# Performance work log

Measured on AMD Instinct MI355X. Metric: run time of the kernel, lower is better.

## Reference

```python
import jax, jax.numpy as jnp
import numpy as np

MARGIN = 1.0   # TripletLoss(margin) init arg
EPS = 1e-6     # torch F.pairwise_distance eps used by nn.TripletMarginLoss
INF = 1e9

N, D_EMB, N_CLASSES = 8192, 1024, 128


def setup_inputs() -> dict:
    key = jax.random.key(0)
    k1, k2 = jax.random.split(key)
    embeddings = jax.random.normal(k1, (N, D_EMB), dtype=jnp.float32)
    target = jax.random.randint(k2, (N,), 0, N_CLASSES, dtype=jnp.int64 if jax.config.jax_enable_x64 else jnp.int32)
    return {"embeddings": embeddings, "target": target}


def _mine_and_loss(embeddings, target):
    # Vectorized, deterministic equivalent of the per-anchor random mining loop:
    # full pairwise L2 distance matrix via a GEMM (compute-bound core).
    sq = jnp.sum(embeddings * embeddings, axis=1)                      # [N]
    d2 = sq[:, None] + sq[None, :] - 2.0 * (embeddings @ embeddings.T)  # [N, N]
    Dm = jnp.sqrt(jnp.maximum(d2, 0.0))                                 # [N, N]

    same = target[:, None] == target[None, :]
    eye = jnp.eye(target.shape[0], dtype=bool)
    pos_mask = same & ~eye          # valid positives (same class, not self)
    neg_mask = ~same                # valid negatives (different class)

    # Positive: hardest (farthest) same-class sample (deterministic stand-in
    # for the original's random positive draw).
    pos_scores = jnp.where(pos_mask, Dm, -INF)
    pos_idx = jnp.argmax(pos_scores, axis=1)                           # [N]
    d_p = jnp.max(pos_scores, axis=1)                                  # [N]

    # Negative: semi-hard (d_p < d_n < d_p + margin), pick the closest such
    # negative; if none exists, fall back to the overall hardest (min-dist)
    # negative -- mirrors the loop's early-break vs. min_dist fallback.
    semi = neg_mask & (Dm > d_p[:, None]) & (Dm < (d_p + MARGIN)[:, None])
    has_semi = jnp.any(semi, axis=1)
    neg_semi = jnp.argmin(jnp.where(semi, Dm, INF), axis=1)
    neg_hard = jnp.argmin(jnp.where(neg_mask, Dm, INF), axis=1)
    neg_idx = jnp.where(has_semi, neg_semi, neg_hard)                  # [N]

    # nn.TripletMarginLoss(margin, p=2): mean(relu(d(a,p) - d(a,n) + margin))
    # with torch's pairwise_distance eps added to the difference.
    a = embeddings
    p = embeddings[pos_idx]
    n = embeddings[neg_idx]
    dp = jnp.sqrt(jnp.sum((a - p + EPS) ** 2, axis=1))
    dn = jnp.sqrt(jnp.sum((a - n + EPS) ** 2, axis=1))
    return jnp.mean(jax.nn.relu(dp - dn + MARGIN))


def reference(embeddings, target):
    return _mine_and_loss(embeddings, target)
```

## Files before the change

### kernel.cpp

```cpp
#include <hip/hip_runtime.h>
#include <hip/hip_bf16.h>

#define N 8192
#define D 1024
#define MARGIN 1.0f
#define EPS 1e-6f

typedef __attribute__((ext_vector_type(8))) short bf16x8;
typedef __attribute__((ext_vector_type(4))) float f32x4;
typedef __attribute__((ext_vector_type(8))) _Float16 f16x8;
typedef __attribute__((ext_vector_type(4))) _Float16 f16x4;
typedef __attribute__((ext_vector_type(8))) unsigned short u16x8;

__device__ inline unsigned short f2bf(float x) {
    unsigned u = __float_as_uint(x);
    unsigned r = (u + 0x7FFFu + ((u >> 16) & 1u)) >> 16;
    return (unsigned short)r;
}

__device__ inline float h2f(unsigned hb) {
    return (float)__builtin_bit_cast(_Float16, (unsigned short)hb);
}

__global__ __launch_bounds__(256) void prep_kernel(const float* __restrict__ E,
                                                   const int* __restrict__ target,
                                                   unsigned short* __restrict__ Ebf,
                                                   float* __restrict__ sq,
                                                   unsigned char* __restrict__ cls) {
    const int tid = threadIdx.x;
    const int lane = tid & 63, wave = tid >> 6;
    const int r = blockIdx.x * 4 + wave;
    const float4 v = ((const float4*)(E + (size_t)r * D))[lane];
    ushort4 o;
    o.x = f2bf(v.x); o.y = f2bf(v.y); o.z = f2bf(v.z); o.w = f2bf(v.w);
    ((ushort4*)(Ebf + (size_t)r * D))[lane] = o;
    float s = v.x * v.x + v.y * v.y + v.z * v.z + v.w * v.w;
    for (int off = 32; off > 0; off >>= 1) s += __shfl_down(s, off);
    if (lane == 0) {
        sq[r] = s;
        cls[r] = (unsigned char)target[r];
    }
}


#define SLOT_0A0 0
#define SLOT_0A1 16384
#define SLOT_0B0 32768
#define SLOT_0B1 49152
#define SLOT_1A0 65536
#define SLOT_1A1 81920
#define SLOT_1B0 98304
#define SLOT_1B1 114688

#define VMW(n) __asm__ __volatile__("s_waitcnt vmcnt(" #n ")" ::: "memory")
#define NOSTAGE ((void)0)
#define NOWAIT ((void)0)

#define STAGE(slotOff, baseRow, kcol) do {                                              \
    const unsigned short* _s0 = E + (size_t)((baseRow) + (tid >> 2)) * D + (kcol) + stc * 8; \
    __builtin_amdgcn_global_load_lds(                                                    \
        (const __attribute__((address_space(1))) unsigned int*)_s0,                      \
        (__attribute__((address_space(3))) unsigned int*)(smem + (slotOff) + wave * 1024), 16, 0, 0); \
    const unsigned short* _s1 = _s0 + (size_t)128 * D;                                   \
    __builtin_amdgcn_global_load_lds(                                                    \
        (const __attribute__((address_space(1))) unsigned int*)_s1,                      \
        (__attribute__((address_space(3))) unsigned int*)(smem + (slotOff) + 8192 + wave * 1024), 16, 0, 0); \
} while (0)

#define PHASE(b, ks, mq, LOADB, STG, WAIT) do {                                          \
    const char* _As = smem + (b) * 65536 + (ks) * 16384;                                 \
    const char* _Bs = smem + (b) * 65536 + 32768 + (ks) * 16384;                         \
    if (LOADB) {                                                                         \
        _Pragma("unroll") for (int nj = 0; nj < 4; ++nj)                                 \
            bfr[nj] = *(const bf16x8*)(_Bs + (wn * 64 + nj * 16 + mr) * 64 + swz);       \
    }                                                                                    \
    bf16x8 af[4];                                                                        \
    _Pragma("unroll") for (int mi = 0; mi < 4; ++mi)                                     \
        af[mi] = *(const bf16x8*)(_As + (wm * 128 + (mq) * 64 + mi * 16 + mr) * 64 + swz); \
    STG;                                                                                 \
    __builtin_amdgcn_s_setprio(1);                                                       \
    _Pragma("unroll") for (int mi = 0; mi < 4; ++mi)                                     \
        _Pragma("unroll") for (int nj = 0; nj < 4; ++nj)                                 \
            acc[(mq) * 4 + mi][nj] = __builtin_amdgcn_mfma_f32_16x16x32_bf16(            \
                af[mi], bfr[nj], acc[(mq) * 4 + mi][nj], 0, 0, 0);                       \
    __builtin_amdgcn_s_setprio(0);                                                       \
    WAIT;                                                                                \
    __asm__ __volatile__("s_barrier" ::: "memory");                                      \
} while (0)

__device__ __forceinline__ void diag_path(char* smem,
                                          const unsigned short* __restrict__ E,
                                          const float* __restrict__ sq,
                                          _Float16* __restrict__ D2h,
                                          const int c, const int tid) {
    const int lane = tid & 63;
    const int wave = tid >> 6;
    const int wmL = wave >> 2;
    const int wnL = wave & 3;
    const int mr = lane & 15;
    const int q = lane >> 4;
    const int kq = q * 8;

    const int t = c / 3, s = c - 3 * t;
    const int smi = (s + 1) >> 1;
    const int sni = s >> 1;
    const int rm = t * 256 + smi * 128;
    const int cn = t * 256 + sni * 128;
    const bool offdiag = (s == 1);

    f32x4 acc[4][2] = {};

#define DSTAGE(sl, kk) do {                                                              \
    __builtin_amdgcn_global_load_lds(                                                    \
        (const __attribute__((address_space(1))) unsigned int*)(E + (size_t)(rm + (tid >> 2)) * D + (kk) * 32 + (tid & 3) * 8), \
        (__attribute__((address_space(3))) unsigned int*)(smem + (sl) * 32768 + wave * 1024), 16, 0, 0); \
    __builtin_amdgcn_global_load_lds(                                                    \
        (const __attribute__((address_space(1))) unsigned int*)(E + (size_t)(cn + (tid >> 2)) * D + (kk) * 32 + (tid & 3) * 8), \
        (__attribute__((address_space(3))) unsigned int*)(smem + (sl) * 32768 + 16384 + wave * 1024), 16, 0, 0); \
} while (0)

#define DCOMPUTE(k) do {                                                                 \
    const unsigned short* As = (const unsigned short*)(smem + (size_t)((k) & 3) * 32768);\
    const unsigned short* Bs = As + 8192;                                                \
    bf16x8 af[4], bfv[2];                                                                \
    _Pragma("unroll") for (int mi = 0; mi < 4; ++mi)                                     \
        af[mi] = *(const bf16x8*)(As + (wmL * 64 + mi * 16 + mr) * 32 + kq);             \
    _Pragma("unroll") for (int ni = 0; ni < 2; ++ni)                                     \
        bfv[ni] = *(const bf16x8*)(Bs + (wnL * 32 + ni * 16 + mr) * 32 + kq);            \
    _Pragma("unroll") for (int mi = 0; mi < 4; ++mi)                                     \
        _Pragma("unroll") for (int ni = 0; ni < 2; ++ni)                                 \
            acc[mi][ni] = __builtin_amdgcn_mfma_f32_16x16x32_bf16(af[mi], bfv[ni], acc[mi][ni], 0, 0, 0); \
} while (0)

    DSTAGE(0, 0);
    DSTAGE(1, 1);
    for (int k = 0; k < 30; ++k) {
        DSTAGE((k + 2) & 3, k + 2);
        __asm__ __volatile__("s_waitcnt vmcnt(4)" ::: "memory");
        __asm__ __volatile__("s_barrier" ::: "memory");
        DCOMPUTE(k);
    }
    __asm__ __volatile__("s_waitcnt vmcnt(2)" ::: "memory");
    __asm__ __volatile__("s_barrier" ::: "memory");
    DCOMPUTE(30);
    __asm__ __volatile__("s_waitcnt vmcnt(0)" ::: "memory");
    __asm__ __volatile__("s_barrier" ::: "memory");
    DCOMPUTE(31);
#undef DSTAGE
#undef DCOMPUTE
    __syncthreads();

    _Float16* Ts = (_Float16*)smem;
    float sqjL[2];
#pragma unroll
    for (int ni = 0; ni < 2; ++ni) sqjL[ni] = sq[cn + wnL * 32 + ni * 16 + mr];
#pragma unroll
    for (int mi = 0; mi < 4; ++mi) {
        const int lrow = wmL * 64 + mi * 16 + q * 4;
        const int i0 = rm + lrow;
        const f32x4 sqi = *(const f32x4*)(sq + i0);
#pragma unroll
        for (int ni = 0; ni < 2; ++ni) {
            const int lcol = wnL * 32 + ni * 16 + mr;
            const int j = cn + lcol;
            f16x4 tv;
#pragma unroll
            for (int r = 0; r < 4; ++r) {
                const float d2 = fmaxf(sqi[r] + sqjL[ni] - 2.0f * acc[mi][ni][r], 0.0f);
                const _Float16 h = (_Float16)d2;
                D2h[(size_t)(i0 + r) * N + j] = h;
                tv[r] = h;
            }
            if (offdiag)
                *(f16x4*)(Ts + (size_t)lcol * 136 + lrow) = tv;
        }
    }
    if (offdiag) {
        __syncthreads();
#pragma unroll
        for (int it = 0; it < 4; ++it) {
            const int rt = it * 32 + (tid >> 4);
            const int seg = tid & 15;
            f16x8 v = *(const f16x8*)(Ts + (size_t)rt * 136 + seg * 8);
            *(f16x8*)(D2h + (size_t)(cn + rt) * N + rm + seg * 8) = v;
        }
    }
}

__global__ __launch_bounds__(512, 2) void gemm_kernel(const unsigned short* __restrict__ E,
                                                      const float* __restrict__ sq,
                                                      _Float16* __restrict__ D2h) {
    extern __shared__ char smem[];

    const int tid = threadIdx.x;

    if (blockIdx.x >= 496) {
        diag_path(smem, E, sq, D2h, blockIdx.x - 496, tid);
        return;
    }

    const int lane = tid & 63;
    const int wave = tid >> 6;
    const int wm = wave >> 2;
    const int wn = wave & 3;
    const int mr = lane & 15;
    const int q = lane >> 4;
    const int swz = ((q ^ ((mr >> 1) & 3)) << 4);
    const int stc = (tid & 3) ^ ((tid >> 3) & 3);

    const int h = blockIdx.x;
    const int l = (h & 7) * 62 + (h >> 3);
    int by = (int)((1.0f + sqrtf(8.0f * (float)l + 1.0f)) * 0.5f);
    while (by * (by - 1) / 2 > l) --by;
    while ((by + 1) * by / 2 <= l) ++by;
    const int bx = l - by * (by - 1) / 2;
    const int rm = by * 256;
    const int cn = bx * 256;

    f32x4 acc[8][4] = {};
    bf16x8 bfr[4];

    STAGE(SLOT_0A0, rm, 0);
    STAGE(SLOT_0B0, cn, 0);
    STAGE(SLOT_0A1, rm, 32);
    STAGE(SLOT_0B1, cn, 32);
    STAGE(SLOT_1A0, rm, 64);
    VMW(6);
    __asm__ __volatile__("s_barrier" ::: "memory");

    for (int i = 0; i < 7; ++i) {
        const int kt = 2 * i;
        PHASE(0, 0, 0, 1, STAGE(SLOT_1B0, cn, (kt + 1) * 64 + 0),  NOWAIT);
        PHASE(0, 0, 1, 0, STAGE(SLOT_1A1, rm, (kt + 1) * 64 + 32), VMW(6));
        PHASE(0, 1, 0, 1, STAGE(SLOT_1B1, cn, (kt + 1) * 64 + 32), NOWAIT);
        PHASE(0, 1, 1, 0, STAGE(SLOT_0A0, rm, (kt + 2) * 64 + 0),  VMW(6));
        PHASE(1, 0, 0, 1, STAGE(SLOT_0B0, cn, (kt + 2) * 64 + 0),  NOWAIT);
        PHASE(1, 0, 1, 0, STAGE(SLOT_0A1, rm, (kt + 2) * 64 + 32), VMW(6));
        PHASE(1, 1, 0, 1, STAGE(SLOT_0B1, cn, (kt + 2) * 64 + 32), NOWAIT);
        PHASE(1, 1, 1, 0, STAGE(SLOT_1A0, rm, (kt + 3) * 64 + 0),  VMW(6));
    }
    PHASE(0, 0, 0, 1, STAGE(SLOT_1B0, cn, 15 * 64 + 0),  NOWAIT);
    PHASE(0, 0, 1, 0, STAGE(SLOT_1A1, rm, 15 * 64 + 32), VMW(6));
    PHASE(0, 1, 0, 1, STAGE(SLOT_1B1, cn, 15 * 64 + 32), NOWAIT);
    PHASE(0, 1, 1, 0, NOSTAGE, VMW(4));
    PHASE(1, 0, 0, 1, NOSTAGE, NOWAIT);
    PHASE(1, 0, 1, 0, NOSTAGE, VMW(0));
    PHASE(1, 1, 0, 1, NOSTAGE, NOWAIT);
    PHASE(1, 1, 1, 0, NOSTAGE, NOWAIT);

    __asm__ __volatile__("s_waitcnt lgkmcnt(0)" ::: "memory");
    __asm__ __volatile__("s_barrier" ::: "memory");

    const int crow = q * 4;
    float sqj[4];
#pragma unroll
    for (int nj = 0; nj < 4; ++nj) sqj[nj] = sq[cn + wn * 64 + nj * 16 + mr];
    float sqiv[8][4];
#pragma unroll
    for (int mg = 0; mg < 8; ++mg) {
        const f32x4 s4 = *(const f32x4*)(sq + rm + wm * 128 + mg * 16 + crow);
#pragma unroll
        for (int r = 0; r < 4; ++r) sqiv[mg][r] = s4[r];
    }

#pragma unroll
    for (int mg = 0; mg < 8; ++mg) {
        const int ilocb = wm * 128 + mg * 16 + crow;
#pragma unroll
        for (int nj = 0; nj < 4; ++nj) {
            const int jloc = wn * 64 + nj * 16 + mr;
            const unsigned jc = (unsigned)jloc >> 3;
            const unsigned jo = ((unsigned)jloc & 7) << 1;
#pragma unroll
            for (int r = 0; r < 4; ++r) {
                const float d2 = fmaxf(sqiv[mg][r] + sqj[nj] - 2.0f * acc[mg][nj][r], 0.0f);
                const int row = ilocb + r;
                *(_Float16*)(smem + (size_t)row * 512 + ((jc ^ (row & 31)) << 4) + jo) = (_Float16)d2;
            }
        }
    }
    __asm__ __volatile__("s_waitcnt lgkmcnt(0)" ::: "memory");
    __asm__ __volatile__("s_barrier" ::: "memory");
    {
        const int seg = tid & 31;
#pragma unroll
        for (int it = 0; it < 16; ++it) {
            const int rt = it * 16 + (tid >> 5);
            f16x8 v = *(const f16x8*)(smem + (size_t)rt * 512 + (((unsigned)seg ^ (rt & 31)) << 4));
            *(f16x8*)(D2h + (size_t)(rm + rt) * N + cn + seg * 8) = v;
        }
    }
    __asm__ __volatile__("s_waitcnt lgkmcnt(0)" ::: "memory");
    __asm__ __volatile__("s_barrier" ::: "memory");

#pragma unroll
    for (int mg = 0; mg < 8; ++mg) {
        const int iloc = wm * 128 + mg * 16 + crow;
        const unsigned cch = (unsigned)iloc >> 3;
        const unsigned cof = ((unsigned)iloc & 7) << 1;
#pragma unroll
        for (int nj = 0; nj < 4; ++nj) {
            const int jloc = wn * 64 + nj * 16 + mr;
            f16x4 tv;
#pragma unroll
            for (int r = 0; r < 4; ++r)
                tv[r] = (_Float16)fmaxf(sqiv[mg][r] + sqj[nj] - 2.0f * acc[mg][nj][r], 0.0f);
            *(f16x4*)(smem + (size_t)jloc * 512 + ((cch ^ (jloc & 31)) << 4) + cof) = tv;
        }
    }
    __asm__ __volatile__("s_waitcnt lgkmcnt(0)" ::: "memory");
    __asm__ __volatile__("s_barrier" ::: "memory");
    {
        const int seg = tid & 31;
#pragma unroll
        for (int it = 0; it < 16; ++it) {
            const int rt = it * 16 + (tid >> 5);
            f16x8 v = *(const f16x8*)(smem + (size_t)rt * 512 + (((unsigned)seg ^ (rt & 31)) << 4));
            *(f16x8*)(D2h + (size_t)(cn + rt) * N + rm + seg * 8) = v;
        }
    }
}

__global__ __launch_bounds__(256) void mine_kernel(const _Float16* __restrict__ D2h,
                                                   const unsigned char* __restrict__ cls,
                                                   float* __restrict__ loss_arr) {
    const int i0 = blockIdx.x * 2;
    const int tid = threadIdx.x;
    const int lane = tid & 63, wave = tid >> 6;
    const unsigned tcbA = cls[i0];
    const unsigned tcbB = cls[i0 + 1];
    const unsigned short* rowA = (const unsigned short*)(D2h + (size_t)i0 * N);
    const unsigned short* rowB = rowA + N;

    u16x8 va[4], vb[4];
    unsigned long long c8[4];
#pragma unroll
    for (int it = 0; it < 4; ++it) {
        va[it] = *(const u16x8*)(rowA + it * 2048 + tid * 8);
        vb[it] = *(const u16x8*)(rowB + it * 2048 + tid * 8);
        c8[it] = *(const unsigned long long*)(cls + it * 2048 + tid * 8);
    }

    unsigned pmA = 0u, nmA = 0xFFFFu, pmB = 0u, nmB = 0xFFFFu;
#pragma unroll
    for (int it = 0; it < 4; ++it) {
#pragma unroll
        for (int e = 0; e < 8; ++e) {
            const unsigned cv = (unsigned)(c8[it] >> (8 * e)) & 0xFFu;
            const unsigned ha = va[it][e];
            const unsigned hb = vb[it][e];
            const bool sA = (cv == tcbA);
            const bool sB = (cv == tcbB);
            pmA = max(pmA, sA ? ha : 0u);
            nmA = min(nmA, sA ? 0xFFFFu : ha);
            pmB = max(pmB, sB ? hb : 0u);
            nmB = min(nmB, sB ? 0xFFFFu : hb);
        }
    }
    for (int off = 1; off < 64; off <<= 1) {
        pmA = max(pmA, (unsigned)__shfl_xor((int)pmA, off));
        nmA = min(nmA, (unsigned)__shfl_xor((int)nmA, off));
        pmB = max(pmB, (unsigned)__shfl_xor((int)pmB, off));
        nmB = min(nmB, (unsigned)__shfl_xor((int)nmB, off));
    }
    __shared__ unsigned redp[2][4], redn[2][4], reds[2][4];
    if (lane == 0) {
        redp[0][wave] = pmA; redn[0][wave] = nmA;
        redp[1][wave] = pmB; redn[1][wave] = nmB;
    }
    __syncthreads();
    pmA = max(max(redp[0][0], redp[0][1]), max(redp[0][2], redp[0][3]));
    nmA = min(min(redn[0][0], redn[0][1]), min(redn[0][2], redn[0][3]));
    pmB = max(max(redp[1][0], redp[1][1]), max(redp[1][2], redp[1][3]));
    nmB = min(min(redn[1][0], redn[1][1]), min(redn[1][2], redn[1][3]));

    unsigned smA = 0xFFFFu, smB = 0xFFFFu;
#pragma unroll
    for (int it = 0; it < 4; ++it) {
#pragma unroll
        for (int e = 0; e < 8; ++e) {
            const unsigned ha = va[it][e];
            const unsigned hb = vb[it][e];
            smA = min(smA, ha > pmA ? ha : 0xFFFFu);
            smB = min(smB, hb > pmB ? hb : 0xFFFFu);
        }
    }
    for (int off = 1; off < 64; off <<= 1) {
        smA = min(smA, (unsigned)__shfl_xor((int)smA, off));
        smB = min(smB, (unsigned)__shfl_xor((int)smB, off));
    }
    if (lane == 0) { reds[0][wave] = smA; reds[1][wave] = smB; }
    __syncthreads();
    if (tid == 0) {
#pragma unroll
        for (int rr = 0; rr < 2; ++rr) {
            const unsigned lob = rr ? pmB : pmA;
            const unsigned nm = rr ? nmB : nmA;
            const unsigned sm = min(min(reds[rr][0], reds[rr][1]),
                                    min(reds[rr][2], reds[rr][3]));
            const float lo = h2f(lob);
            const float dp = sqrtf(lo);
            const float hw = dp + MARGIN;
            const float hi = hw * hw;
            const float smv = h2f(sm);
            const float dn2 = (smv < hi) ? smv : h2f(nm);
            loss_arr[i0 + rr] = fmaxf(dp - sqrtf(dn2) + MARGIN, 0.0f);
        }
    }
}

__global__ __launch_bounds__(256) void reduce_kernel(const float* __restrict__ loss_arr,
                                                     float* __restrict__ out) {
    const int tid = threadIdx.x;
    float s = 0.0f;
    for (int k = tid; k < N; k += 256) s += loss_arr[k];
    for (int off = 32; off > 0; off >>= 1) s += __shfl_down(s, off);
    __shared__ float red[4];
    const int lane = tid & 63, wave = tid >> 6;
    if (lane == 0) red[wave] = s;
    __syncthreads();
    if (tid == 0) out[0] = (red[0] + red[1] + red[2] + red[3]) * (1.0f / N);
}

extern "C" void kernel_launch(void* const* d_in, const int* in_sizes, int n_in,
                              void* d_out, int out_size, void* d_ws, size_t ws_size,
                              hipStream_t stream) {
    const float* E = (const float*)d_in[0];
    const int* target = (const int*)d_in[1];
    float* out = (float*)d_out;
    char* ws = (char*)d_ws;

    unsigned short* Ebf = (unsigned short*)ws;
    float* sq        = (float*)(ws + (size_t)16777216);
    float* loss_arr  = (float*)(ws + (size_t)16809984);
    unsigned char* cls = (unsigned char*)(ws + (size_t)16842752);
    _Float16* D2h    = (_Float16*)(ws + (size_t)16875520);

    static bool attr_set = false;
    if (!attr_set) {
        hipFuncSetAttribute((const void*)gemm_kernel,
                            hipFuncAttributeMaxDynamicSharedMemorySize, 131072);
        attr_set = true;
    }

    prep_kernel<<<N / 4, 256, 0, stream>>>(E, target, Ebf, sq, cls);
    gemm_kernel<<<592, 512, 131072, stream>>>(Ebf, sq, D2h);
    mine_kernel<<<N / 2, 256, 0, stream>>>(D2h, cls, loss_arr);
    reduce_kernel<<<1, 256, 0, stream>>>(loss_arr, out);
}
```

Before: 185.4 us.

## Deepen GEMM load prefetch schedule and fuse loss reduction via atomics

The GEMM main loop's staging schedule is reorganised. One extra B stage is prefetched in the prologue, loads are issued in pairs in later phases, and wait points move so more global-to-LDS traffic stays in flight per MFMA phase. Separately, the final reduce kernel is removed: the output is zeroed in prep_kernel and each mine block atomically adds its scaled partial loss. This saves one kernel launch and a global round trip, at the cost of 4096 float atomics and a summation order that is no longer deterministic.

```diff
diff --git a/kernel.cpp b/kernel.cpp
--- a/kernel.cpp
+++ b/kernel.cpp
@@ -26,10 +26,12 @@
                                                    const int* __restrict__ target,
                                                    unsigned short* __restrict__ Ebf,
                                                    float* __restrict__ sq,
-                                                   unsigned char* __restrict__ cls) {
+                                                   unsigned char* __restrict__ cls,
+                                                   float* __restrict__ out) {
     const int tid = threadIdx.x;
     const int lane = tid & 63, wave = tid >> 6;
     const int r = blockIdx.x * 4 + wave;
+    if (blockIdx.x == 0 && tid == 0) out[0] = 0.0f;
     const float4 v = ((const float4*)(E + (size_t)r * D))[lane];
     ushort4 o;
     o.x = f2bf(v.x); o.y = f2bf(v.y); o.z = f2bf(v.z); o.w = f2bf(v.w);
@@ -66,6 +68,8 @@
         (const __attribute__((address_space(1))) unsigned int*)_s1,                      \
         (__attribute__((address_space(3))) unsigned int*)(smem + (slotOff) + 8192 + wave * 1024), 16, 0, 0); \
 } while (0)
+
+#define STAGE2(s1, b1, k1, s2, b2, k2) do { STAGE(s1, b1, k1); STAGE(s2, b2, k2); } while (0)
 
 #define PHASE(b, ks, mq, LOADB, STG, WAIT) do {                                          \
     const char* _As = smem + (b) * 65536 + (ks) * 16384;                                 \
@@ -225,26 +229,29 @@
     STAGE(SLOT_0A1, rm, 32);
     STAGE(SLOT_0B1, cn, 32);
     STAGE(SLOT_1A0, rm, 64);
-    VMW(6);
+    STAGE(SLOT_1B0, cn, 64);
+    VMW(4);
     __asm__ __volatile__("s_barrier" ::: "memory");
 
     for (int i = 0; i < 7; ++i) {
         const int kt = 2 * i;
-        PHASE(0, 0, 0, 1, STAGE(SLOT_1B0, cn, (kt + 1) * 64 + 0),  NOWAIT);
-        PHASE(0, 0, 1, 0, STAGE(SLOT_1A1, rm, (kt + 1) * 64 + 32), VMW(6));
-        PHASE(0, 1, 0, 1, STAGE(SLOT_1B1, cn, (kt + 1) * 64 + 32), NOWAIT);
-        PHASE(0, 1, 1, 0, STAGE(SLOT_0A0, rm, (kt + 2) * 64 + 0),  VMW(6));
-        PHASE(1, 0, 0, 1, STAGE(SLOT_0B0, cn, (kt + 2) * 64 + 0),  NOWAIT);
-        PHASE(1, 0, 1, 0, STAGE(SLOT_0A1, rm, (kt + 2) * 64 + 32), VMW(6));
-        PHASE(1, 1, 0, 1, STAGE(SLOT_0B1, cn, (kt + 2) * 64 + 32), NOWAIT);
-        PHASE(1, 1, 1, 0, STAGE(SLOT_1A0, rm, (kt + 3) * 64 + 0),  VMW(6));
-    }
-    PHASE(0, 0, 0, 1, STAGE(SLOT_1B0, cn, 15 * 64 + 0),  NOWAIT);
-    PHASE(0, 0, 1, 0, STAGE(SLOT_1A1, rm, 15 * 64 + 32), VMW(6));
-    PHASE(0, 1, 0, 1, STAGE(SLOT_1B1, cn, 15 * 64 + 32), NOWAIT);
-    PHASE(0, 1, 1, 0, NOSTAGE, VMW(4));
+        PHASE(0, 0, 0, 1, STAGE(SLOT_1A1, rm, (kt + 1) * 64 + 32), NOWAIT);
+        PHASE(0, 0, 1, 0, STAGE(SLOT_1B1, cn, (kt + 1) * 64 + 32), NOWAIT);
+        PHASE(0, 1, 0, 1, STAGE(SLOT_0A0, rm, (kt + 2) * 64 + 0),  NOWAIT);
+        PHASE(0, 1, 1, 0, STAGE(SLOT_0B0, cn, (kt + 2) * 64 + 0),  VMW(4));
+        PHASE(1, 0, 0, 1, STAGE2(SLOT_0A1, rm, (kt + 2) * 64 + 32,
+                                 SLOT_0B1, cn, (kt + 2) * 64 + 32), NOWAIT);
+        PHASE(1, 0, 1, 0, NOSTAGE, NOWAIT);
+        PHASE(1, 1, 0, 1, STAGE2(SLOT_1A0, rm, (kt + 3) * 64 + 0,
+                                 SLOT_1B0, cn, (kt + 3) * 64 + 0),  NOWAIT);
+        PHASE(1, 1, 1, 0, NOSTAGE, VMW(4));
+    }
+    PHASE(0, 0, 0, 1, STAGE(SLOT_1A1, rm, 15 * 64 + 32), NOWAIT);
+    PHASE(0, 0, 1, 0, STAGE(SLOT_1B1, cn, 15 * 64 + 32), NOWAIT);
+    PHASE(0, 1, 0, 1, NOSTAGE, NOWAIT);
+    PHASE(0, 1, 1, 0, NOSTAGE, VMW(0));
     PHASE(1, 0, 0, 1, NOSTAGE, NOWAIT);
-    PHASE(1, 0, 1, 0, NOSTAGE, VMW(0));
+    PHASE(1, 0, 1, 0, NOSTAGE, NOWAIT);
     PHASE(1, 1, 0, 1, NOSTAGE, NOWAIT);
     PHASE(1, 1, 1, 0, NOSTAGE, NOWAIT);
 
@@ -323,7 +330,7 @@
 
 __global__ __launch_bounds__(256) void mine_kernel(const _Float16* __restrict__ D2h,
                                                    const unsigned char* __restrict__ cls,
-                                                   float* __restrict__ loss_arr) {
+                                                   float* __restrict__ out) {
     const int i0 = blockIdx.x * 2;
     const int tid = threadIdx.x;
     const int lane = tid & 63, wave = tid >> 6;
@@ -392,6 +399,7 @@
     if (lane == 0) { reds[0][wave] = smA; reds[1][wave] = smB; }
     __syncthreads();
     if (tid == 0) {
+        float acc = 0.0f;
 #pragma unroll
         for (int rr = 0; rr < 2; ++rr) {
             const unsigned lob = rr ? pmB : pmA;
@@ -404,22 +412,10 @@
             const float hi = hw * hw;
             const float smv = h2f(sm);
             const float dn2 = (smv < hi) ? smv : h2f(nm);
-            loss_arr[i0 + rr] = fmaxf(dp - sqrtf(dn2) + MARGIN, 0.0f);
-        }
-    }
-}
-
-__global__ __launch_bounds__(256) void reduce_kernel(const float* __restrict__ loss_arr,
-                                                     float* __restrict__ out) {
-    const int tid = threadIdx.x;
-    float s = 0.0f;
-    for (int k = tid; k < N; k += 256) s += loss_arr[k];
-    for (int off = 32; off > 0; off >>= 1) s += __shfl_down(s, off);
-    __shared__ float red[4];
-    const int lane = tid & 63, wave = tid >> 6;
-    if (lane == 0) red[wave] = s;
-    __syncthreads();
-    if (tid == 0) out[0] = (red[0] + red[1] + red[2] + red[3]) * (1.0f / N);
+            acc += fmaxf(dp - sqrtf(dn2) + MARGIN, 0.0f);
+        }
+        atomicAdd(out, acc * (1.0f / N));
+    }
 }
 
 extern "C" void kernel_launch(void* const* d_in, const int* in_sizes, int n_in,
@@ -432,7 +428,6 @@
 
     unsigned short* Ebf = (unsigned short*)ws;
     float* sq        = (float*)(ws + (size_t)16777216);
-    float* loss_arr  = (float*)(ws + (size_t)16809984);
     unsigned char* cls = (unsigned char*)(ws + (size_t)16842752);
     _Float16* D2h    = (_Float16*)(ws + (size_t)16875520);
 
@@ -443,8 +438,7 @@
         attr_set = true;
     }
 
-    prep_kernel<<<N / 4, 256, 0, stream>>>(E, target, Ebf, sq, cls);
+    prep_kernel<<<N / 4, 256, 0, stream>>>(E, target, Ebf, sq, cls, out);
     gemm_kernel<<<592, 512, 131072, stream>>>(Ebf, sq, D2h);
-    mine_kernel<<<N / 2, 256, 0, stream>>>(D2h, cls, loss_arr);
-    reduce_kernel<<<1, 256, 0, stream>>>(loss_arr, out);
-}
+    mine_kernel<<<N / 2, 256, 0, stream>>>(D2h, cls, out);
+}
```

After: 214.7 us. 1.16x slower.
